# Kernel tuning notes

Hardware: AMD Instinct MI355X
Metric: run time of the kernel (lower is better)

Reference implementation:

```python
import jax, jax.numpy as jnp
import numpy as np

H = 1024   # HIDDEN_DIM
V = 15000  # VOCAB_SIZE
L = 2      # NUM_LAYERS
E = 4      # experts per block
B, S = 32, 2048


def rmsnorm(x, w, eps=1e-6):
    return x * jax.lax.rsqrt(jnp.mean(x * x, axis=-1, keepdims=True) + eps) * w


def setup_inputs() -> dict:
    key = jax.random.key(0)
    ks = jax.random.split(key, 8)
    windows = jax.random.randint(ks[0], (B, S), 0, V, dtype=jnp.int32)
    hemis = jax.random.randint(ks[1], (B,), 0, 2, dtype=jnp.int32)
    experts = jax.random.randint(ks[2], (B,), 0, E, dtype=jnp.int32)
    emb = jax.random.normal(ks[3], (V, H), dtype=jnp.float32) * 0.02
    norm1_w = jnp.ones((L, H), dtype=jnp.float32)
    decay_logit = jnp.full((L, H), 2.0, dtype=jnp.float32)  # torch init: ones*2.0
    norm2_w = jnp.ones((L, H), dtype=jnp.float32)
    # expert weights, torch Linear layout [out, in] per expert: [L, E, H, H]
    Wexp = jax.random.normal(ks[4], (L, E, H, H), dtype=jnp.float32) * 0.02
    final_norm_w = jnp.ones((H,), dtype=jnp.float32)
    lm_head = jax.random.normal(ks[5], (V, H), dtype=jnp.float32) * 0.02
    return dict(windows=windows, hemis=hemis, experts=experts, emb=emb,
                norm1_w=norm1_w, decay_logit=decay_logit, norm2_w=norm2_w,
                Wexp=Wexp, final_norm_w=final_norm_w, lm_head=lm_head)


def reference(windows, hemis, experts, emb, norm1_w, decay_logit, norm2_w,
              Wexp, final_norm_w, lm_head):
    del hemis  # only used for router loss when targets are given (inference path)
    x = emb[windows]  # [B,S,H]
    onehot = jax.nn.one_hot(experts, E, dtype=x.dtype)  # [B,E]
    for l in range(L):
        xn = rmsnorm(x, norm1_w[l])
        decay = jax.nn.sigmoid(decay_logit[l])  # [H]

        def step(state, xt):
            s = state * decay + xt * (1.0 - decay)
            return s, s

        init = jnp.zeros((x.shape[0], H), dtype=x.dtype)
        _, states = jax.lax.scan(step, init, jnp.swapaxes(xn, 0, 1))  # [S,B,H]
        x = x + jnp.swapaxes(states, 0, 1)
        pool = rmsnorm(x, norm2_w[l])[:, -1, :]  # [B,H]
        # all 4 expert FFNs on the pooled state, then select by expert id
        out_all = jax.nn.relu(jnp.einsum('bh,edh->ebd', pool, Wexp[l]))  # [E,B,H]
        out = jnp.einsum('be,ebh->bh', onehot, out_all)  # [B,H]
        x = x + out[:, None, :]
    final_state = rmsnorm(x[:, -1, :], final_norm_w)
    logits = final_state @ lm_head.T  # [B,V]
    return logits
```

## Files before the change

kernel.cpp:

```cpp
#include <hip/hip_runtime.h>
#include <cstddef>
#include <cstdint>

#define H 1024
#define V 15000
#define NE 4
#define B 32
#define S 2048
#define EPS 1e-6f
#define CH 32
#define T0 64
#define SB 8
#define NVT 938

typedef unsigned short u16;
typedef __attribute__((ext_vector_type(8))) short bf16x8;
typedef __attribute__((ext_vector_type(4))) float f32x4;

__device__ __forceinline__ float wave_sum(float x) {
#pragma unroll
  for (int off = 32; off > 0; off >>= 1) x += __shfl_down(x, off);
  return x;
}

__device__ __forceinline__ float bf2f(u16 u) {
  union { uint32_t i; float f; } x;
  x.i = ((uint32_t)u) << 16;
  return x.f;
}

__device__ __forceinline__ float bflo(uint32_t u) {
  union { uint32_t i; float f; } x;
  x.i = u << 16;
  return x.f;
}
__device__ __forceinline__ float bfhi(uint32_t u) {
  union { uint32_t i; float f; } x;
  x.i = u & 0xFFFF0000u;
  return x.f;
}

__device__ __forceinline__ u16 f2bf(float f) {
  union { float f; uint32_t i; } x;
  x.f = f;
  const uint32_t u = x.i;
  return (u16)((u + 0x7FFFu + ((u >> 16) & 1u)) >> 16);
}

__device__ __forceinline__ float uasf(uint32_t u) {
  union { uint32_t i; float f; } x;
  x.i = u;
  return x.f;
}
__device__ __forceinline__ uint32_t fasu(float f) {
  union { float f; uint32_t i; } x;
  x.f = f;
  return x.i;
}

__device__ __forceinline__ void split2(float x0, float x1, uint32_t& hp,
                                       uint32_t& lp) {
  const uint32_t u0 = fasu(x0), u1 = fasu(x1);
  hp = (u0 >> 16) | (u1 & 0xFFFF0000u);
  const float l0 = x0 - uasf(u0 & 0xFFFF0000u);
  const float l1 = x1 - uasf(u1 & 0xFFFF0000u);
  asm("v_cvt_pk_bf16_f32 %0, %1, %2" : "=v"(lp) : "v"(l0), "v"(l1));
}

__global__ __launch_bounds__(256) void k_vocab(const float* __restrict__ emb,
                                               float* __restrict__ invr1,
                                               u16* __restrict__ embh) {
  const int gw = (blockIdx.x * blockDim.x + threadIdx.x) >> 6;
  const int lane = threadIdx.x & 63;
  if (gw >= V) return;
  const float4* row = (const float4*)(emb + (size_t)gw * H);
  float s = 0.f;
#pragma unroll
  for (int j = 0; j < 4; ++j) {
    const float4 f = row[lane + 64 * j];
    s += f.x * f.x + f.y * f.y + f.z * f.z + f.w * f.w;
    if (embh) {
      ushort4 h4;
      h4.x = f2bf(f.x); h4.y = f2bf(f.y); h4.z = f2bf(f.z); h4.w = f2bf(f.w);
      ((ushort4*)(embh + (size_t)gw * H))[lane + 64 * j] = h4;
    }
  }
  s = wave_sum(s);
  if (lane == 0) invr1[gw] = rsqrtf(s * (1.f / H) + EPS);
}

__global__ void k_bucket(const int* __restrict__ experts,
                         int* __restrict__ elist, int* __restrict__ ecnt) {
  if (threadIdx.x == 0 && blockIdx.x == 0) {
    int c[NE] = {0, 0, 0, 0};
    for (int b = 0; b < B; ++b) {
      const int e = experts[b];
      elist[e * B + c[e]] = b;
      c[e]++;
    }
    for (int e = 0; e < NE; ++e) ecnt[e] = c[e];
  }
}

template <int BF>
__global__ __launch_bounds__(512, 8) void k_scanA(
    const int* __restrict__ windows, const float* __restrict__ emb,
    const u16* __restrict__ embh, const float* __restrict__ norm1_w,
    const float* __restrict__ decay_logit, const float* __restrict__ invr1,
    float* __restrict__ local1) {
  __shared__ int tok_l[T0];
  __shared__ float iv_l[T0];
  const int b = blockIdx.x / CH, c = blockIdx.x % CH;
  const int tid = threadIdx.x;
  const int h2 = tid * 2;
  if (tid < T0) {
    const int tok = windows[b * S + c * T0 + tid];
    tok_l[tid] = tok << 10;
    iv_l[tid] = invr1[tok];
  }
  const float d1a = 1.f / (1.f + expf(-decay_logit[h2]));
  const float d1b = 1.f / (1.f + expf(-decay_logit[h2 + 1]));
  const float g1a = norm1_w[h2] * (1.f - d1a);
  const float g1b = norm1_w[h2 + 1] * (1.f - d1b);
  __syncthreads();
  float sa = 0.f, sbv = 0.f;
  for (int t0 = 0; t0 < T0; t0 += SB) {
    uint32_t u[SB];
    float2 ef[SB];
#pragma unroll
    for (int k = 0; k < SB; ++k) {
      if constexpr (BF)
        u[k] = *(const uint32_t*)(embh + (size_t)(tok_l[t0 + k] + h2));
      else
        ef[k] = *(const float2*)(emb + (size_t)(tok_l[t0 + k] + h2));
    }
#pragma unroll
    for (int k = 0; k < SB; ++k) {
      const float iv = iv_l[t0 + k];
      const float ea = BF ? bflo(u[k]) : ef[k].x;
      const float eb = BF ? bfhi(u[k]) : ef[k].y;
      sa = sa * d1a + ea * (iv * g1a);
      sbv = sbv * d1b + eb * (iv * g1b);
    }
  }
  *(float2*)(local1 + (size_t)(b * CH + c) * H + h2) = make_float2(sa, sbv);
}

__global__ __launch_bounds__(1024) void k_scanB(
    const int* __restrict__ windows, const float* __restrict__ emb,
    const float* __restrict__ decay_logit, const float* __restrict__ local1,
    float* __restrict__ s1start, float* __restrict__ es1,
    float* __restrict__ invp) {
  __shared__ float red[16];
  const int b = blockIdx.x, h = threadIdx.x;
  const float d1 = 1.f / (1.f + expf(-decay_logit[h]));
  float dT = d1;
#pragma unroll
  for (int i = 0; i < 6; ++i) dT *= dT;
  float Sv = 0.f;
  for (int c = 0; c < CH; ++c) {
    const size_t idx = (size_t)(b * CH + c) * H + h;
    s1start[idx] = Sv;
    Sv = dT * Sv + local1[idx];
  }
  const int tl = windows[b * S + S - 1];
  const float v = emb[(size_t)tl * H + h] + Sv;
  es1[b * H + h] = v;
  const float q = wave_sum(v * v);
  if ((h & 63) == 0) red[h >> 6] = q;
  __syncthreads();
  if (h == 0) {
    float t = 0.f;
#pragma unroll
    for (int i = 0; i < 16; ++i) t += red[i];
    invp[b] = rsqrtf(t * (1.f / H) + EPS);
  }
}

__global__ __launch_bounds__(256) void k_expert2(
    const float* __restrict__ src, const float* __restrict__ invp,
    const float* __restrict__ n2w, const float* __restrict__ Wl,
    const int* __restrict__ elist, const int* __restrict__ ecnt,
    float* __restrict__ outp) {
  const int e = blockIdx.x >> 6;
  const int dgrp = blockIdx.x & 63;
  const int cnt = ecnt[e];
  if (cnt == 0) return;
  const int wave = threadIdx.x >> 6, lane = threadIdx.x & 63;
  const float* W = Wl + (size_t)e * H * H;
  const float4* n2w4 = (const float4*)n2w;
#pragma unroll 1
  for (int i = 0; i < 4; ++i) {
    const int dd = dgrp * 16 + wave * 4 + i;
    const float4* wr4 = (const float4*)(W + (size_t)dd * H);
    float4 w4[4];
#pragma unroll
    for (int j = 0; j < 4; ++j) w4[j] = wr4[lane + 64 * j];
#pragma unroll 1
    for (int bi = 0; bi < cnt; ++bi) {
      const int b = elist[e * B + bi];
      const float4* s4 = (const float4*)(src + b * H);
      float s = 0.f;
#pragma unroll
      for (int j = 0; j < 4; ++j) {
        const float4 sv = s4[lane + 64 * j];
        const float4 nv = n2w4[lane + 64 * j];
        s += w4[j].x * sv.x * nv.x + w4[j].y * sv.y * nv.y +
             w4[j].z * sv.z * nv.z + w4[j].w * sv.w * nv.w;
      }
      s = wave_sum(s);
      if (lane == 0) outp[b * H + dd] = fmaxf(s * invp[b], 0.f);
    }
  }
}

template <int BF>
__global__ __launch_bounds__(512, 8) void k_fuseCD(
    const int* __restrict__ windows, const float* __restrict__ emb,
    const u16* __restrict__ embh, const float* __restrict__ norm1_w,
    const float* __restrict__ decay_logit, const float* __restrict__ invr1,
    const float* __restrict__ s1start, const float* __restrict__ out1,
    float* __restrict__ local2, float* __restrict__ x1last) {
  __shared__ int tok_l[T0];
  __shared__ float iv_l[T0];
  __shared__ float sq[SB][512];
  __shared__ float rinv_l[SB];
  const int b = blockIdx.x / CH, c = blockIdx.x % CH;
  const int tid = threadIdx.x;
  const int h2 = 2 * tid;
  if (tid < T0) {
    const int tok = windows[b * S + c * T0 + tid];
    tok_l[tid] = tok << 10;
    iv_l[tid] = invr1[tok];
  }
  const float d1a = 1.f / (1.f + expf(-decay_logit[h2]));
  const float d1b = 1.f / (1.f + expf(-decay_logit[h2 + 1]));
  const float g1a = norm1_w[h2] * (1.f - d1a);
  const float g1b = norm1_w[h2 + 1] * (1.f - d1b);
  const float d2a = 1.f / (1.f + expf(-decay_logit[H + h2]));
  const float d2b = 1.f / (1.f + expf(-decay_logit[H + h2 + 1]));
  const float g2a = norm1_w[H + h2] * (1.f - d2a);
  const float g2b = norm1_w[H + h2 + 1] * (1.f - d2b);
  const float2 o1 = *(const float2*)(out1 + b * H + h2);
  const float2 s1v = *(const float2*)(s1start + (size_t)(b * CH + c) * H + h2);
  float s1a = s1v.x, s1b = s1v.y;
  float s2a = 0.f, s2b = 0.f;
  __syncthreads();
  const int wv = tid >> 6, lane = tid & 63;
  float x1a[SB], x1b[SB];
  for (int sb = 0; sb < T0 / SB; ++sb) {
    uint32_t u[SB];
    float2 ef[SB];
#pragma unroll
    for (int k = 0; k < SB; ++k) {
      const int t = sb * SB + k;
      if constexpr (BF)
        u[k] = *(const uint32_t*)(embh + (size_t)(tok_l[t] + h2));
      else
        ef[k] = *(const float2*)(emb + (size_t)(tok_l[t] + h2));
    }
#pragma unroll
    for (int k = 0; k < SB; ++k) {
      const float iv = iv_l[sb * SB + k];
      const float ea = BF ? bflo(u[k]) : ef[k].x;
      const float eb = BF ? bfhi(u[k]) : ef[k].y;
      s1a = s1a * d1a + ea * (iv * g1a);
      s1b = s1b * d1b + eb * (iv * g1b);
      x1a[k] = ea + s1a + o1.x;
      x1b[k] = eb + s1b + o1.y;
      sq[k][tid] = x1a[k] * x1a[k] + x1b[k] * x1b[k];
    }
    __syncthreads();
    float ssum = 0.f;
#pragma unroll
    for (int j = 0; j < 8; ++j) ssum += sq[wv][lane + 64 * j];
    ssum = wave_sum(ssum);
    if (lane == 0) rinv_l[wv] = rsqrtf(ssum * (1.f / H) + EPS);
    __syncthreads();
#pragma unroll
    for (int k = 0; k < SB; ++k) {
      const float ra = rinv_l[k];
      s2a = s2a * d2a + x1a[k] * (ra * g2a);
      s2b = s2b * d2b + x1b[k] * (ra * g2b);
    }
  }
  *(float2*)(local2 + (size_t)(b * CH + c) * H + h2) = make_float2(s2a, s2b);
  if (c == CH - 1)
    *(float2*)(x1last + b * H + h2) = make_float2(x1a[SB - 1], x1b[SB - 1]);
}

__global__ __launch_bounds__(1024) void k_scanE(
    const float* __restrict__ decay_logit, const float* __restrict__ local2,
    const float* __restrict__ x1last, float* __restrict__ es2,
    float* __restrict__ invp) {
  __shared__ float red[16];
  const int b = blockIdx.x, h = threadIdx.x;
  const float d2 = 1.f / (1.f + expf(-decay_logit[H + h]));
  float dT = d2;
#pragma unroll
  for (int i = 0; i < 6; ++i) dT *= dT;
  float Sv = 0.f;
  for (int c = 0; c < CH; ++c)
    Sv = dT * Sv + local2[(size_t)(b * CH + c) * H + h];
  const float v = x1last[b * H + h] + Sv;
  es2[b * H + h] = v;
  const float q = wave_sum(v * v);
  if ((h & 63) == 0) red[h >> 6] = q;
  __syncthreads();
  if (h == 0) {
    float t = 0.f;
#pragma unroll
    for (int i = 0; i < 16; ++i) t += red[i];
    invp[32 + b] = rsqrtf(t * (1.f / H) + EPS);
  }
}

__global__ __launch_bounds__(256) void k_fstate(const float* __restrict__ es2,
    const float* __restrict__ out2, const float* __restrict__ fnw,
    u16* __restrict__ fsth, u16* __restrict__ fstl) {
  __shared__ float red[4];
  const int b = blockIdx.x, tid = threadIdx.x;
  float4 x = ((const float4*)(es2 + b * H))[tid];
  const float4 y = ((const float4*)(out2 + b * H))[tid];
  x.x += y.x; x.y += y.y; x.z += y.z; x.w += y.w;
  float s = x.x * x.x + x.y * x.y + x.z * x.z + x.w * x.w;
  s = wave_sum(s);
  if ((tid & 63) == 0) red[tid >> 6] = s;
  __syncthreads();
  const float ir =
      rsqrtf((red[0] + red[1] + red[2] + red[3]) * (1.f / H) + EPS);
  const float4 w = ((const float4*)fnw)[tid];
  float o[4];
  o[0] = x.x * ir * w.x; o[1] = x.y * ir * w.y;
  o[2] = x.z * ir * w.z; o[3] = x.w * ir * w.w;
  ushort4 hs, ls;
  u16* hp = (u16*)&hs;
  u16* lp = (u16*)&ls;
#pragma unroll
  for (int j = 0; j < 4; ++j) {
    const uint32_t u = fasu(o[j]);
    hp[j] = (u16)(u >> 16);
    lp[j] = f2bf(o[j] - uasf(u & 0xFFFF0000u));
  }
  ((ushort4*)(fsth + b * H))[tid] = hs;
  ((ushort4*)(fstl + b * H))[tid] = ls;
}

__global__ __launch_bounds__(256) void k_logits(const float* __restrict__ lm,
    const u16* __restrict__ fsth, const u16* __restrict__ fstl,
    float* __restrict__ outp) {
  __shared__ float red[4][2][4][64];
  const int tid = threadIdx.x;
  const int w = tid >> 6, l = tid & 63;
  const int ln = l & 15, kg = l >> 4;
  const int v0 = blockIdx.x * 16;
  int r = v0 + ln;
  if (r > V - 1) r = V - 1;
  const int kbase = w * 256 + kg * 8;
  const float* lrow = lm + (size_t)r * H + kbase;
  const u16* fh0 = fsth + (size_t)ln * H + kbase;
  const u16* fh1 = fsth + (size_t)(16 + ln) * H + kbase;
  const u16* fl0 = fstl + (size_t)ln * H + kbase;
  const u16* fl1 = fstl + (size_t)(16 + ln) * H + kbase;
  f32x4 acc0 = {0.f, 0.f, 0.f, 0.f};
  f32x4 acc1 = {0.f, 0.f, 0.f, 0.f};
#pragma unroll 1
  for (int it = 0; it < 8; ++it) {
    const int ko = it * 32;
    const float4 xa = *(const float4*)(lrow + ko);
    const float4 xb = *(const float4*)(lrow + ko + 4);
    union { bf16x8 v; uint32_t u[4]; } Bh, Bl, Ah0, Ah1, Al0, Al1;
    split2(xa.x, xa.y, Bh.u[0], Bl.u[0]);
    split2(xa.z, xa.w, Bh.u[1], Bl.u[1]);
    split2(xb.x, xb.y, Bh.u[2], Bl.u[2]);
    split2(xb.z, xb.w, Bh.u[3], Bl.u[3]);
    *(uint4*)Ah0.u = *(const uint4*)(fh0 + ko);
    *(uint4*)Ah1.u = *(const uint4*)(fh1 + ko);
    *(uint4*)Al0.u = *(const uint4*)(fl0 + ko);
    *(uint4*)Al1.u = *(const uint4*)(fl1 + ko);
    acc0 = __builtin_amdgcn_mfma_f32_16x16x32_bf16(Ah0.v, Bh.v, acc0, 0, 0, 0);
    acc1 = __builtin_amdgcn_mfma_f32_16x16x32_bf16(Ah1.v, Bh.v, acc1, 0, 0, 0);
    acc0 = __builtin_amdgcn_mfma_f32_16x16x32_bf16(Ah0.v, Bl.v, acc0, 0, 0, 0);
    acc1 = __builtin_amdgcn_mfma_f32_16x16x32_bf16(Ah1.v, Bl.v, acc1, 0, 0, 0);
    acc0 = __builtin_amdgcn_mfma_f32_16x16x32_bf16(Al0.v, Bh.v, acc0, 0, 0, 0);
    acc1 = __builtin_amdgcn_mfma_f32_16x16x32_bf16(Al1.v, Bh.v, acc1, 0, 0, 0);
  }
#pragma unroll
  for (int q = 0; q < 4; ++q) {
    red[w][0][q][l] = acc0[q];
    red[w][1][q][l] = acc1[q];
  }
  __syncthreads();
  const int rr = tid >> 6, lane2 = tid & 63;
  const int vv = v0 + (lane2 & 15);
  if (vv < V) {
#pragma unroll
    for (int mt = 0; mt < 2; ++mt) {
      const float s = red[0][mt][rr][lane2] + red[1][mt][rr][lane2] +
                      red[2][mt][rr][lane2] + red[3][mt][rr][lane2];
      const int bb = mt * 16 + 4 * (lane2 >> 4) + rr;
      outp[(size_t)bb * V + vv] = s;
    }
  }
}

extern "C" void kernel_launch(void* const* d_in, const int* in_sizes, int n_in,
                              void* d_out, int out_size, void* d_ws,
                              size_t ws_size, hipStream_t stream) {
  const int* windows = (const int*)d_in[0];
  const int* experts = (const int*)d_in[2];
  const float* emb = (const float*)d_in[3];
  const float* norm1_w = (const float*)d_in[4];
  const float* decay_logit = (const float*)d_in[5];
  const float* norm2_w = (const float*)d_in[6];
  const float* Wexp = (const float*)d_in[7];
  const float* final_norm_w = (const float*)d_in[8];
  const float* lm_head = (const float*)d_in[9];
  float* outp = (float*)d_out;

  float* ws = (float*)d_ws;
  float* invr1 = ws;
  float* local1 = invr1 + 15360;
  float* s1start = local1 + B * CH * H;
  float* local2 = s1start + B * CH * H;
  float* out1 = local2 + B * CH * H;
  float* out2 = out1 + B * H;
  float* es1 = out2 + B * H;
  float* es2 = es1 + B * H;
  float* x1last = es2 + B * H;
  float* invp = x1last + B * H;
  int* elist = (int*)(invp + 64);
  int* ecnt = elist + NE * B;
  u16* fsth = (u16*)(ecnt + NE);
  u16* fstl = fsth + B * H;
  u16* embh = (u16*)(((uintptr_t)(fstl + B * H) + 255) & ~(uintptr_t)255);
  const size_t need = (size_t)((char*)embh - (char*)d_ws) + (size_t)V * H * 2;
  const bool use_bf = ws_size >= need;

  k_vocab<<<(V * 64 + 255) / 256, 256, 0, stream>>>(emb, invr1,
                                                    use_bf ? embh : nullptr);
  k_bucket<<<1, 64, 0, stream>>>(experts, elist, ecnt);
  if (use_bf)
    k_scanA<1><<<B * CH, 512, 0, stream>>>(windows, emb, embh, norm1_w,
                                           decay_logit, invr1, local1);
  else
    k_scanA<0><<<B * CH, 512, 0, stream>>>(windows, emb, embh, norm1_w,
                                           decay_logit, invr1, local1);
  k_scanB<<<B, 1024, 0, stream>>>(windows, emb, decay_logit, local1, s1start,
                                  es1, invp);
  k_expert2<<<NE * 64, 256, 0, stream>>>(es1, invp, norm2_w, Wexp, elist,
                                         ecnt, out1);
  if (use_bf)
    k_fuseCD<1><<<B * CH, 512, 0, stream>>>(windows, emb, embh, norm1_w,
                                            decay_logit, invr1, s1start,
                                            out1, local2, x1last);
  else
    k_fuseCD<0><<<B * CH, 512, 0, stream>>>(windows, emb, embh, norm1_w,
                                            decay_logit, invr1, s1start,
                                            out1, local2, x1last);
  k_scanE<<<B, 1024, 0, stream>>>(decay_logit, local2, x1last, es2, invp);
  k_expert2<<<NE * 64, 256, 0, stream>>>(es2, invp + 32, norm2_w + H,
                                         Wexp + (size_t)NE * H * H, elist,
                                         ecnt, out2);
  k_fstate<<<B, 256, 0, stream>>>(es2, out2, final_norm_w, fsth, fstl);
  k_logits<<<NVT, 256, 0, stream>>>(lm_head, fsth, fstl, outp);
}
```

Before: 303.0 us.

## Stage lm_head tile into LDS via direct global-to-LDS loads, prefetch activations into registers

The logits kernel now copies each block's 16 lm_head rows into padded shared memory using global_load_lds with coalesced 16-byte per-lane transfers, instead of each lane striding through rows with scattered float4 loads. It also preloads all final-state hi/lo bf16 fragments into registers before the barrier, fully unrolls the k loop, and sets launch bounds to 2 blocks per CU. The aim is coalesced HBM access and overlapping all loads up front, at the cost of about 66KB of LDS per block and higher register pressure, which may limit occupancy.

Result: faster. 294.2 us (-2.9%).

```diff
diff --git a/kernel.cpp b/kernel.cpp
--- a/kernel.cpp
+++ b/kernel.cpp
@@ -12,6 +12,7 @@
 #define T0 64
 #define SB 8
 #define NVT 938
+#define LMP 1028
 
 typedef unsigned short u16;
 typedef __attribute__((ext_vector_type(8))) short bf16x8;
@@ -56,6 +57,10 @@
   union { float f; uint32_t i; } x;
   x.f = f;
   return x.i;
+}
+
+__device__ __forceinline__ void pinu4(const uint4& v) {
+  asm volatile("" :: "v"(v.x), "v"(v.y), "v"(v.z), "v"(v.w));
 }
 
 __device__ __forceinline__ void split2(float x0, float x1, uint32_t& hp,
@@ -346,38 +351,70 @@
   ((ushort4*)(fstl + b * H))[tid] = ls;
 }
 
-__global__ __launch_bounds__(256) void k_logits(const float* __restrict__ lm,
+__global__ __launch_bounds__(256, 2) void k_logits(const float* __restrict__ lm,
     const u16* __restrict__ fsth, const u16* __restrict__ fstl,
     float* __restrict__ outp) {
+  __shared__ float lmt[16 * LMP];
   __shared__ float red[4][2][4][64];
   const int tid = threadIdx.x;
   const int w = tid >> 6, l = tid & 63;
   const int ln = l & 15, kg = l >> 4;
   const int v0 = blockIdx.x * 16;
-  int r = v0 + ln;
-  if (r > V - 1) r = V - 1;
-  const int kbase = w * 256 + kg * 8;
-  const float* lrow = lm + (size_t)r * H + kbase;
-  const u16* fh0 = fsth + (size_t)ln * H + kbase;
-  const u16* fh1 = fsth + (size_t)(16 + ln) * H + kbase;
-  const u16* fl0 = fstl + (size_t)ln * H + kbase;
-  const u16* fl1 = fstl + (size_t)(16 + ln) * H + kbase;
+  const int kq = w * 256;
+
+  const u16* fh0 = fsth + (size_t)ln * H + kq + kg * 8;
+  const u16* fh1 = fsth + (size_t)(16 + ln) * H + kq + kg * 8;
+  const u16* fl0 = fstl + (size_t)ln * H + kq + kg * 8;
+  const u16* fl1 = fstl + (size_t)(16 + ln) * H + kq + kg * 8;
+  uint4 Hf0[8], Hf1[8], Lf0[8], Lf1[8];
+#pragma unroll
+  for (int j = 0; j < 8; ++j) {
+    Hf0[j] = *(const uint4*)(fh0 + j * 32);
+    Hf1[j] = *(const uint4*)(fh1 + j * 32);
+    Lf0[j] = *(const uint4*)(fl0 + j * 32);
+    Lf1[j] = *(const uint4*)(fl1 + j * 32);
+  }
+
+#pragma unroll
+  for (int i = 0; i < 4; ++i) {
+    const int rr = w + 4 * i;
+    int r = v0 + rr;
+    if (r > V - 1) r = V - 1;
+    const float* gsrc = lm + (size_t)r * H + l * 4;
+#pragma unroll
+    for (int c = 0; c < 4; ++c) {
+      __builtin_amdgcn_global_load_lds(
+          (const __attribute__((address_space(1))) uint32_t*)(gsrc + c * 256),
+          (__attribute__((address_space(3))) uint32_t*)&lmt[rr * LMP + c * 256],
+          16, 0, 0);
+    }
+  }
+#pragma unroll
+  for (int j = 0; j < 8; ++j) {
+    pinu4(Hf0[j]); pinu4(Hf1[j]); pinu4(Lf0[j]); pinu4(Lf1[j]);
+  }
+  __syncthreads();
+
   f32x4 acc0 = {0.f, 0.f, 0.f, 0.f};
   f32x4 acc1 = {0.f, 0.f, 0.f, 0.f};
-#pragma unroll 1
-  for (int it = 0; it < 8; ++it) {
-    const int ko = it * 32;
-    const float4 xa = *(const float4*)(lrow + ko);
-    const float4 xb = *(const float4*)(lrow + ko + 4);
+  const float* lrow = &lmt[ln * LMP + kq + kg * 8];
+#pragma unroll
+  for (int j = 0; j < 8; ++j) {
+    const float4 xa = *(const float4*)(lrow + j * 32);
+    const float4 xb = *(const float4*)(lrow + j * 32 + 4);
     union { bf16x8 v; uint32_t u[4]; } Bh, Bl, Ah0, Ah1, Al0, Al1;
     split2(xa.x, xa.y, Bh.u[0], Bl.u[0]);
     split2(xa.z, xa.w, Bh.u[1], Bl.u[1]);
     split2(xb.x, xb.y, Bh.u[2], Bl.u[2]);
     split2(xb.z, xb.w, Bh.u[3], Bl.u[3]);
-    *(uint4*)Ah0.u = *(const uint4*)(fh0 + ko);
-    *(uint4*)Ah1.u = *(const uint4*)(fh1 + ko);
-    *(uint4*)Al0.u = *(const uint4*)(fl0 + ko);
-    *(uint4*)Al1.u = *(const uint4*)(fl1 + ko);
+    Ah0.u[0] = Hf0[j].x; Ah0.u[1] = Hf0[j].y;
+    Ah0.u[2] = Hf0[j].z; Ah0.u[3] = Hf0[j].w;
+    Ah1.u[0] = Hf1[j].x; Ah1.u[1] = Hf1[j].y;
+    Ah1.u[2] = Hf1[j].z; Ah1.u[3] = Hf1[j].w;
+    Al0.u[0] = Lf0[j].x; Al0.u[1] = Lf0[j].y;
+    Al0.u[2] = Lf0[j].z; Al0.u[3] = Lf0[j].w;
+    Al1.u[0] = Lf1[j].x; Al1.u[1] = Lf1[j].y;
+    Al1.u[2] = Lf1[j].z; Al1.u[3] = Lf1[j].w;
     acc0 = __builtin_amdgcn_mfma_f32_16x16x32_bf16(Ah0.v, Bh.v, acc0, 0, 0, 0);
     acc1 = __builtin_amdgcn_mfma_f32_16x16x32_bf16(Ah1.v, Bh.v, acc1, 0, 0, 0);
     acc0 = __builtin_amdgcn_mfma_f32_16x16x32_bf16(Ah0.v, Bl.v, acc0, 0, 0, 0);
@@ -385,6 +422,7 @@
     acc0 = __builtin_amdgcn_mfma_f32_16x16x32_bf16(Al0.v, Bh.v, acc0, 0, 0, 0);
     acc1 = __builtin_amdgcn_mfma_f32_16x16x32_bf16(Al1.v, Bh.v, acc1, 0, 0, 0);
   }
+
 #pragma unroll
   for (int q = 0; q < 4; ++q) {
     red[w][0][q][l] = acc0[q];
```
